# Kernel optimization log

Hardware: AMD Instinct MI355X
Metric: run time of the kernel (lower is better)

The kernel has to match this reference:

```python
import jax, jax.numpy as jnp
import numpy as np

N_NODES = 100000
N_EDGES = 1000000
F_IN = 8
HID = 64
VOCAB = 64
TXT_F = 64
SEQ = 10
N_CLASSES = 2


def setup_inputs() -> dict:
    key = jax.random.key(0)
    ks = jax.random.split(key, 16)
    inp = {
        "x": jax.random.normal(ks[0], (N_NODES, F_IN), dtype=jnp.float32),
        "edge_index": jax.random.randint(ks[1], (2, N_EDGES), 0, N_NODES, dtype=jnp.int32),
        "xtext": jax.random.randint(ks[2], (N_NODES, SEQ), 0, VOCAB, dtype=jnp.int32),
        # GCN layers (PyG convention: out = norm_agg(x @ W) + b)
        "conv1_w": jax.random.normal(ks[3], (F_IN, HID), dtype=jnp.float32) * 0.2,
        "conv1_b": jnp.zeros((HID,), jnp.float32),
        "conv2_w": jax.random.normal(ks[4], (HID, HID), dtype=jnp.float32) * 0.1,
        "conv2_b": jnp.zeros((HID,), jnp.float32),
        # embedding + GRU (torch layout: w_ih [3H, in], w_hh [3H, H])
        "embed": jax.random.normal(ks[5], (VOCAB, TXT_F), dtype=jnp.float32) * 0.1,
        "gru_w_ih": jax.random.normal(ks[6], (3 * HID, TXT_F), dtype=jnp.float32) * 0.1,
        "gru_w_hh": jax.random.normal(ks[7], (3 * HID, HID), dtype=jnp.float32) * 0.1,
        "gru_b_ih": jnp.zeros((3 * HID,), jnp.float32),
        "gru_b_hh": jnp.zeros((3 * HID,), jnp.float32),
        # pair MLPs (torch Linear layout: [out, in])
        "lin1_w": jax.random.normal(ks[8], (HID, 2 * HID), dtype=jnp.float32) * 0.1,
        "lin1_b": jnp.zeros((HID,), jnp.float32),
        "lin_text_w": jax.random.normal(ks[9], (HID, 2 * HID), dtype=jnp.float32) * 0.1,
        "lin_text_b": jnp.zeros((HID,), jnp.float32),
        "lin_final_w": jax.random.normal(ks[10], (N_CLASSES, 2 * HID), dtype=jnp.float32) * 0.1,
        "lin_final_b": jnp.zeros((N_CLASSES,), jnp.float32),
    }
    return inp


def _gcn_norm(edge_index, n_nodes):
    # PyG GCNConv default: add self loops, symmetric normalization
    loops = jnp.arange(n_nodes, dtype=edge_index.dtype)
    src = jnp.concatenate([edge_index[0], loops])
    dst = jnp.concatenate([edge_index[1], loops])
    deg = jax.ops.segment_sum(jnp.ones_like(dst, dtype=jnp.float32), dst, num_segments=n_nodes)
    dinv = jnp.where(deg > 0, jax.lax.rsqrt(deg), 0.0)
    norm = dinv[src] * dinv[dst]  # [E+N]
    return src, dst, norm


def _gcn(h, src, dst, norm, W, b, n_nodes):
    h = h @ W                              # [N, out]
    msg = h[src] * norm[:, None]           # gather + scale
    out = jax.ops.segment_sum(msg, dst, num_segments=n_nodes)
    return out + b


def _gru_last(xe, w_ih, w_hh, b_ih, b_hh):
    # xe: [N, T, F]; returns last hidden state [N, H]
    H = w_hh.shape[1]
    gi_all = jnp.einsum('ntf,gf->ntg', xe, w_ih) + b_ih  # precompute input gates [N,T,3H]
    gi_all = jnp.transpose(gi_all, (1, 0, 2))            # [T, N, 3H]

    def step(h, gi):
        gh = h @ w_hh.T + b_hh
        i_r, i_z, i_n = jnp.split(gi, 3, axis=-1)
        h_r, h_z, h_n = jnp.split(gh, 3, axis=-1)
        r = jax.nn.sigmoid(i_r + h_r)
        z = jax.nn.sigmoid(i_z + h_z)
        n = jnp.tanh(i_n + r * h_n)
        h = (1.0 - z) * n + z * h
        return h, None

    h0 = jnp.zeros((xe.shape[0], H), xe.dtype)
    h_last, _ = jax.lax.scan(step, h0, gi_all)
    return h_last


def reference(x, edge_index, xtext,
              conv1_w, conv1_b, conv2_w, conv2_b,
              embed, gru_w_ih, gru_w_hh, gru_b_ih, gru_b_hh,
              lin1_w, lin1_b, lin_text_w, lin_text_b, lin_final_w, lin_final_b):
    n = x.shape[0]
    src, dst, norm = _gcn_norm(edge_index, n)

    h = jax.nn.relu(_gcn(x, src, dst, norm, conv1_w, conv1_b, n))
    h = jax.nn.relu(_gcn(h, src, dst, norm, conv2_w, conv2_b, n))

    xe = embed[xtext]                                   # [N, T, F]
    textout = _gru_last(xe, gru_w_ih, gru_w_hh, gru_b_ih, gru_b_hh)  # [N, 64]

    s, t = edge_index[0], edge_index[1]
    xpair = jnp.concatenate([h[s], h[t]], axis=1)       # [E, 128]
    xpair = jax.nn.relu(xpair @ lin1_w.T + lin1_b)

    xpairtext = jnp.concatenate([textout[s], textout[t]], axis=1)
    xpairtext = jax.nn.relu(xpairtext @ lin_text_w.T + lin_text_b)

    xfin = jnp.concatenate([xpair, xpairtext], axis=1) @ lin_final_w.T + lin_final_b
    return jax.nn.log_softmax(xfin, axis=1)
```

## Files before the change

### kernel.cpp

```cpp
#include <hip/hip_runtime.h>
#include <stdint.h>

#define N_NODES 100000
#define N_EDGES 1000000
#define NBLK 391

typedef unsigned short u16;
typedef unsigned int u32;
typedef __attribute__((ext_vector_type(8))) short bshort8;
typedef __attribute__((ext_vector_type(4))) float f32x4;

__device__ __forceinline__ float bf2f(u16 u){ union{float f; u32 i;} x; x.i=((u32)u)<<16; return x.f; }
__device__ __forceinline__ u16 f2bf(float f){ union{float f; u32 i;} x; x.f=f; u32 r = x.i + 0x7FFFu + ((x.i>>16)&1u); return (u16)(r>>16); }

__device__ __forceinline__ float fexp2(float x){
#if __has_builtin(__builtin_amdgcn_exp2f)
    return __builtin_amdgcn_exp2f(x);
#else
    return exp2f(x);
#endif
}
__device__ __forceinline__ float frcp(float x){
#if __has_builtin(__builtin_amdgcn_rcpf)
    return __builtin_amdgcn_rcpf(x);
#else
    return 1.0f/x;
#endif
}
#define LOG2E 1.442695041f

__global__ void k_detect(const u16* __restrict__ x, int* flagp){
    __shared__ int cnt;
    if(threadIdx.x == 0) cnt = 0;
    __syncthreads();
    int c = 0;
    for(int i = threadIdx.x; i < 2048; i += 256){
        int e = (x[i] >> 7) & 0xFF;
        if(e >= 0x90) c++;
    }
    atomicAdd(&cnt, c);
    __syncthreads();
    if(threadIdx.x == 0) flagp[0] = (cnt > 64) ? 1 : 0;
}

#define CX    0
#define CW1   800000
#define CB1   800512
#define CW2   800576
#define CB2   804672
#define CEMB  804736
#define CWIH  808832
#define CWHH  821120
#define CBIH  833408
#define CBHH  833600
#define CL1W  833792
#define CL1B  841984
#define CLTW  842048
#define CLTB  850240
#define CLFW  850304
#define CLFB  850560
#define CTOT  850562

__device__ __forceinline__ float ldany(const void* p, int i, int fl){
    return fl ? ((const float*)p)[i] : bf2f(((const u16*)p)[i]);
}

__global__ void k_convert(const int* __restrict__ flagp,
                          const void* x, const void* w1, const void* b1, const void* w2,
                          const void* b2, const void* emb, const void* wih, const void* whh,
                          const void* bih, const void* bhh, const void* l1w, const void* l1b,
                          const void* ltw, const void* ltb, const void* lfw, const void* lfb,
                          float* __restrict__ canon){
    int i = blockIdx.x*256 + threadIdx.x;
    if(i >= CTOT) return;
    int fl = *flagp;
    const void* p; int off;
    if     (i < CW1 ){ p = x;   off = i;        }
    else if(i < CB1 ){ p = w1;  off = i - CW1;  }
    else if(i < CW2 ){ p = b1;  off = i - CB1;  }
    else if(i < CB2 ){ p = w2;  off = i - CW2;  }
    else if(i < CEMB){ p = b2;  off = i - CB2;  }
    else if(i < CWIH){ p = emb; off = i - CEMB; }
    else if(i < CWHH){ p = wih; off = i - CWIH; }
    else if(i < CBIH){ p = whh; off = i - CWHH; }
    else if(i < CBHH){ p = bih; off = i - CBIH; }
    else if(i < CL1W){ p = bhh; off = i - CBHH; }
    else if(i < CL1B){ p = l1w; off = i - CL1W; }
    else if(i < CLTW){ p = l1b; off = i - CL1B; }
    else if(i < CLTB){ p = ltw; off = i - CLTW; }
    else if(i < CLFW){ p = ltb; off = i - CLTB; }
    else if(i < CLFB){ p = lfw; off = i - CLFW; }
    else             { p = lfb; off = i - CLFB; }
    float v = ldany(p, off, fl);
    canon[i] = (v == v && fabsf(v) < 1e30f) ? v : 0.f;
}

__global__ void k_hist(const int* __restrict__ ei, int* __restrict__ deg){
    int e = blockIdx.x*256 + threadIdx.x;
    if(e < N_EDGES) atomicAdd(&deg[ei[N_EDGES + e]], 1);
}
__global__ void k_scan1(const int* __restrict__ deg, int* __restrict__ rowptr,
                        int* __restrict__ bsum){
    __shared__ int sh[256];
    int tid = threadIdx.x;
    int i = blockIdx.x*256 + tid;
    int v = (i < N_NODES) ? deg[i] : 0;
    sh[tid] = v;
    __syncthreads();
    for(int off = 1; off < 256; off <<= 1){
        int t = (tid >= off) ? sh[tid - off] : 0;
        __syncthreads();
        sh[tid] += t;
        __syncthreads();
    }
    if(i < N_NODES) rowptr[i] = sh[tid] - v;
    if(tid == 255) bsum[blockIdx.x] = sh[255];
}
__global__ void k_scan2(int* __restrict__ bsum){
    __shared__ int sh[512];
    int tid = threadIdx.x;
    int v = (tid < NBLK) ? bsum[tid] : 0;
    sh[tid] = v;
    __syncthreads();
    for(int off = 1; off < 512; off <<= 1){
        int t = (tid >= off) ? sh[tid - off] : 0;
        __syncthreads();
        sh[tid] += t;
        __syncthreads();
    }
    if(tid < NBLK) bsum[tid] = sh[tid] - v;
}
__global__ void k_scan3(const int* __restrict__ deg, const int* __restrict__ bsum,
                        int* __restrict__ rowptr, int* __restrict__ cursor,
                        float* __restrict__ dinv){
    int i = blockIdx.x*256 + threadIdx.x;
    if(i < N_NODES){
        int r = rowptr[i] + bsum[i >> 8];
        rowptr[i] = r;
        cursor[i] = r;
        dinv[i] = rsqrtf((float)deg[i] + 1.0f);
    }
    if(i == 0) rowptr[N_NODES] = N_EDGES;
}
__global__ void k_fill(const int* __restrict__ ei, int* __restrict__ cursor,
                       int* __restrict__ el, int* __restrict__ dl, int* __restrict__ eid){
    int e = blockIdx.x*256 + threadIdx.x;
    if(e < N_EDGES){
        int s = ei[e], d = ei[N_EDGES + e];
        int pos = atomicAdd(&cursor[d], 1);
        el[pos] = s;
        dl[pos] = d;
        eid[pos] = e;
    }
}

__global__ void k_t1s(const float* __restrict__ cx, const float* __restrict__ cw1,
                      const float* __restrict__ dinv, u16* __restrict__ src){
    __shared__ float w[512];
    int t = threadIdx.x;
    w[t]       = cw1[t];
    w[t + 256] = cw1[t + 256];
    __syncthreads();
    int i = blockIdx.x*256 + t;
    int n = i >> 6, f = i & 63;
    const float* xr = cx + n*8;
    float acc = 0.f;
    #pragma unroll
    for(int k = 0; k < 8; k++) acc += xr[k] * w[k*64 + f];
    src[i] = f2bf(acc * dinv[n]);
}

__global__ __launch_bounds__(256)
void k_gather_ep(const int* __restrict__ rowptr, const int* __restrict__ el,
                 const u16* __restrict__ src, const float* __restrict__ dinv,
                 const float* __restrict__ b, u16* __restrict__ h, int ostride){
    int gid = blockIdx.x*256 + threadIdx.x;
    int node = gid >> 6, lane = gid & 63;
    int beg = rowptr[node], end = rowptr[node + 1];
    float acc = bf2f(src[node*64 + lane]);
    int i = beg;
    for(; i + 4 <= end; i += 4){
        int s0 = el[i], s1 = el[i+1], s2 = el[i+2], s3 = el[i+3];
        float a0 = bf2f(src[s0*64 + lane]);
        float a1 = bf2f(src[s1*64 + lane]);
        float a2 = bf2f(src[s2*64 + lane]);
        float a3 = bf2f(src[s3*64 + lane]);
        acc += a0; acc += a1; acc += a2; acc += a3;
    }
    for(; i < end; i++) acc += bf2f(src[el[i]*64 + lane]);
    h[node*ostride + lane] = f2bf(fmaxf(dinv[node]*acc + b[lane], 0.f));
}

__global__ void k_packb(const float* __restrict__ src, u16* __restrict__ dst,
                        int K, int N, int ldk, int ldn){
    int i = blockIdx.x*256 + threadIdx.x;
    if(i >= K*N) return;
    int k = i / N, n = i % N;
    int kt = k >> 5, kk = k & 31, q = kk >> 3, j = kk & 7;
    int nt = n >> 4, nn = n & 15;
    int KT = K >> 5;
    dst[(((nt*KT + kt)*64) + (q*16 + nn))*8 + j] = f2bf(src[k*ldk + n*ldn]);
}

__global__ void k_gitab(const float* __restrict__ emb, const float* __restrict__ wih,
                        const float* __restrict__ bih, const float* __restrict__ bhh,
                        float* __restrict__ giT){
    int i = blockIdx.x*256 + threadIdx.x;
    if(i >= 64*192) return;
    int v = i / 192, g = i % 192;
    float acc = bih[g] + ((g < 128) ? bhh[g] : 0.0f);
    const float* wr = wih + g*64;
    const float* er = emb + v*64;
    for(int f = 0; f < 64; f++) acc += wr[f] * er[f];
    int g3 = g >> 6, rem = g & 63, t = rem >> 4, col = rem & 15;
    giT[(((size_t)v*3 + g3)*16 + col)*4 + t] = acc;
}

__global__ __launch_bounds__(256, 4)
void k_conv2(const u16* __restrict__ h, const u16* __restrict__ w2p,
             const float* __restrict__ dinv, u16* __restrict__ src){
    int wv = threadIdx.x >> 6, lane = threadIdx.x & 63;
    int g = blockIdx.x*4 + wv;
    if(g >= N_NODES/16) return;
    int q = lane >> 4, m = lane & 15, col = m;
    bshort8 a0 = *(const bshort8*)(h + (g*16 + m)*64 + q*8);
    bshort8 a1 = *(const bshort8*)(h + (g*16 + m)*64 + 32 + q*8);
    f32x4 acc[4];
    #pragma unroll
    for(int nt = 0; nt < 4; nt++){
        f32x4 c = {0.f,0.f,0.f,0.f};
        c = __builtin_amdgcn_mfma_f32_16x16x32_bf16(a0, *(const bshort8*)(w2p + ((nt*2+0)*64 + lane)*8), c, 0,0,0);
        c = __builtin_amdgcn_mfma_f32_16x16x32_bf16(a1, *(const bshort8*)(w2p + ((nt*2+1)*64 + lane)*8), c, 0,0,0);
        acc[nt] = c;
    }
    #pragma unroll
    for(int nt = 0; nt < 4; nt++)
        #pragma unroll
        for(int r = 0; r < 4; r++){
            int node = g*16 + q*4 + r;
            src[node*64 + nt*16 + col] = f2bf(acc[nt][r] * dinv[node]);
        }
}

__global__ __launch_bounds__(256, 4)
void k_gru(const int* __restrict__ xt, const u16* __restrict__ whhp,
           const float* __restrict__ giT, const float* __restrict__ bhh,
           u16* __restrict__ txt){
    __shared__ __align__(16) u16 wsh[12288];
    __shared__ __align__(16) u16 hsh[4][16][72];
    int tid = threadIdx.x;
    {
        const uint4* s = (const uint4*)whhp;
        uint4* d = (uint4*)wsh;
        #pragma unroll
        for(int i = 0; i < 6; i++) d[tid + 256*i] = s[tid + 256*i];
    }
    __syncthreads();

    int wv = tid >> 6, lane = tid & 63;
    int q = lane >> 4, m = lane & 15, col = m;
    int g = blockIdx.x*4 + wv;
    bool active = g < (N_NODES/16);
    int nb = active ? g*16 : 0;

    float bhhn[4];
    #pragma unroll
    for(int t = 0; t < 4; t++) bhhn[t] = bhh[128 + t*16 + col];

    const bshort8* wl = (const bshort8*)wsh;
    const u16* hp = &hsh[wv][m][0];

    float hc[4][4];
    #pragma unroll
    for(int t = 0; t < 4; t++)
        #pragma unroll
        for(int r = 0; r < 4; r++) hc[t][r] = 0.f;

    for(int s = 0; s < 10; s++){
        #pragma unroll
        for(int t = 0; t < 4; t++)
            #pragma unroll
            for(int r = 0; r < 4; r++)
                hsh[wv][q*4 + r][t*16 + col] = f2bf(hc[t][r]);

        asm volatile("" ::: "memory");
        bshort8 a0 = *(const bshort8*)(hp + q*8);
        bshort8 a1 = *(const bshort8*)(hp + 32 + q*8);

        int tok[4];
        #pragma unroll
        for(int r = 0; r < 4; r++) tok[r] = xt[(nb + q*4 + r)*10 + s] & 63;

        f32x4 acc[12];
        #pragma unroll
        for(int nt = 0; nt < 12; nt++){
            f32x4 c = {0.f,0.f,0.f,0.f};
            c = __builtin_amdgcn_mfma_f32_16x16x32_bf16(a0, wl[(nt*2+0)*64 + lane], c, 0,0,0);
            c = __builtin_amdgcn_mfma_f32_16x16x32_bf16(a1, wl[(nt*2+1)*64 + lane], c, 0,0,0);
            acc[nt] = c;
        }

        #pragma unroll
        for(int r = 0; r < 4; r++){
            const float4* gp = (const float4*)(giT + (size_t)tok[r]*192);
            float4 gr = gp[col];
            float4 gz = gp[16 + col];
            float4 gn = gp[32 + col];
            #pragma unroll
            for(int t = 0; t < 4; t++){
                float gir = ((const float*)&gr)[t];
                float giz = ((const float*)&gz)[t];
                float gin = ((const float*)&gn)[t];
                float rr = frcp(1.0f + fexp2(-LOG2E*(gir + acc[t][r])));
                float zz = frcp(1.0f + fexp2(-LOG2E*(giz + acc[4+t][r])));
                float narg = gin + rr*(acc[8+t][r] + bhhn[t]);
                float e2 = fexp2(2.0f*LOG2E*narg);
                float nn = 1.0f - 2.0f*frcp(e2 + 1.0f);
                hc[t][r] = nn + zz*(hc[t][r] - nn);
            }
        }
        asm volatile("" ::: "memory");
    }
    if(active){
        #pragma unroll
        for(int t = 0; t < 4; t++)
            #pragma unroll
            for(int r = 0; r < 4; r++)
                txt[(size_t)(nb + q*4 + r)*128 + t*16 + col] = f2bf(hc[t][r]);
    }
}

__global__ __launch_bounds__(256, 3)
void k_pairpre(u16* nodef, u32* __restrict__ udst,
               const u16* __restrict__ w1a, const u16* __restrict__ w1b,
               const u16* __restrict__ wta, const u16* __restrict__ wtb,
               const float* __restrict__ b1, const float* __restrict__ bt){
    int wv = threadIdx.x >> 6, lane = threadIdx.x & 63;
    int g = blockIdx.x*4 + wv;
    if(g >= N_NODES/16) return;
    int q = lane >> 4, m = lane & 15, col = m;
    const u16* row = nodef + (size_t)(g*16 + m)*128;
    bshort8 ah0 = *(const bshort8*)(row + q*8);
    bshort8 ah1 = *(const bshort8*)(row + 32 + q*8);
    bshort8 at0 = *(const bshort8*)(row + 64 + q*8);
    bshort8 at1 = *(const bshort8*)(row + 96 + q*8);
    f32x4 u1[4], u2[4], v1[4], v2[4];
    #pragma unroll
    for(int nt = 0; nt < 4; nt++){
        f32x4 c;
        c = (f32x4){0.f,0.f,0.f,0.f};
        c = __builtin_amdgcn_mfma_f32_16x16x32_bf16(ah0, *(const bshort8*)(w1a + ((nt*2+0)*64 + lane)*8), c, 0,0,0);
        c = __builtin_amdgcn_mfma_f32_16x16x32_bf16(ah1, *(const bshort8*)(w1a + ((nt*2+1)*64 + lane)*8), c, 0,0,0);
        u1[nt] = c;
        c = (f32x4){0.f,0.f,0.f,0.f};
        c = __builtin_amdgcn_mfma_f32_16x16x32_bf16(ah0, *(const bshort8*)(w1b + ((nt*2+0)*64 + lane)*8), c, 0,0,0);
        c = __builtin_amdgcn_mfma_f32_16x16x32_bf16(ah1, *(const bshort8*)(w1b + ((nt*2+1)*64 + lane)*8), c, 0,0,0);
        u2[nt] = c;
        c = (f32x4){0.f,0.f,0.f,0.f};
        c = __builtin_amdgcn_mfma_f32_16x16x32_bf16(at0, *(const bshort8*)(wta + ((nt*2+0)*64 + lane)*8), c, 0,0,0);
        c = __builtin_amdgcn_mfma_f32_16x16x32_bf16(at1, *(const bshort8*)(wta + ((nt*2+1)*64 + lane)*8), c, 0,0,0);
        v1[nt] = c;
        c = (f32x4){0.f,0.f,0.f,0.f};
        c = __builtin_amdgcn_mfma_f32_16x16x32_bf16(at0, *(const bshort8*)(wtb + ((nt*2+0)*64 + lane)*8), c, 0,0,0);
        c = __builtin_amdgcn_mfma_f32_16x16x32_bf16(at1, *(const bshort8*)(wtb + ((nt*2+1)*64 + lane)*8), c, 0,0,0);
        v2[nt] = c;
    }
    u32* usrc = (u32*)nodef;
    #pragma unroll
    for(int nt = 0; nt < 4; nt++){
        int f = nt*16 + col;
        float b1f = b1[f], btf = bt[f];
        #pragma unroll
        for(int r = 0; r < 4; r++){
            int node = g*16 + q*4 + r;
            u32 pa = (u32)f2bf(u1[nt][r] + b1f) | ((u32)f2bf(v1[nt][r] + btf) << 16);
            u32 pb = (u32)f2bf(u2[nt][r]) | ((u32)f2bf(v2[nt][r]) << 16);
            usrc[(size_t)node*64 + f] = pa;
            udst[(size_t)node*64 + f] = pb;
        }
    }
}

__global__ __launch_bounds__(256, 6)
void k_edge2(const int* __restrict__ el, const int* __restrict__ dl, const int* __restrict__ eid,
             const u32* __restrict__ usrc, const u32* __restrict__ udst,
             const float* __restrict__ wfin, const float* __restrict__ bfin,
             const int* __restrict__ flagp, void* __restrict__ out){
    int tid = threadIdx.x;
    int lane = tid & 63;
    int q = lane >> 4, f0 = lane & 15;
    int wid = (blockIdx.x*256 + tid) >> 6;
    int nwv = (gridDim.x*256) >> 6;
    int fl = *flagp;

    float wp0[4], wp1[4], wt0[4], wt1[4];
    #pragma unroll
    for(int t = 0; t < 4; t++){
        int f = f0 + 16*t;
        wp0[t] = wfin[f];        wt0[t] = wfin[64 + f];
        wp1[t] = wfin[128 + f];  wt1[t] = wfin[192 + f];
    }
    float bf0 = bfin[0], bf1 = bfin[1];

    for(int grp = wid; grp < N_EDGES/4; grp += nwv){
        int e = grp*4 + q;
        int s = el[e], d = dl[e];
        const u32* up = usrc + (size_t)s*64 + f0;
        const u32* vp = udst + (size_t)d*64 + f0;
        u32 us[4], ud[4];
        #pragma unroll
        for(int t = 0; t < 4; t++){ us[t] = up[16*t]; ud[t] = vp[16*t]; }
        float s0 = 0.f, s1 = 0.f;
        #pragma unroll
        for(int t = 0; t < 4; t++){
            float u1 = __uint_as_float(us[t] << 16);
            float v1 = __uint_as_float(us[t] & 0xffff0000u);
            float u2 = __uint_as_float(ud[t] << 16);
            float v2 = __uint_as_float(ud[t] & 0xffff0000u);
            float xp = fmaxf(u1 + u2, 0.f);
            float xq = fmaxf(v1 + v2, 0.f);
            s0 += xp*wp0[t] + xq*wt0[t];
            s1 += xp*wp1[t] + xq*wt1[t];
        }
        #pragma unroll
        for(int msk = 1; msk < 16; msk <<= 1){
            s0 += __shfl_xor(s0, msk, 64);
            s1 += __shfl_xor(s1, msk, 64);
        }
        if(f0 == 0){
            float a = s0 + bf0, b = s1 + bf1;
            float mx = fmaxf(a, b);
            float lse = mx + __logf(__expf(a - mx) + __expf(b - mx));
            int oi = eid[e];
            if(fl){
                float2 v; v.x = a - lse; v.y = b - lse;
                ((float2*)out)[oi] = v;
            }else{
                u32 pack = (u32)f2bf(a - lse) | ((u32)f2bf(b - lse) << 16);
                ((u32*)out)[oi] = pack;
            }
        }
    }
}

static const size_t O_FLAG   = 0;
static const size_t O_CANON  = 4096;
static const size_t O_GIT    = 3407872;
static const size_t O_W2P    = 3457024;
static const size_t O_WHHP   = 3465216;
static const size_t O_L1PA   = 3489792;
static const size_t O_L1PB   = 3497984;
static const size_t O_LTPA   = 3506176;
static const size_t O_LTPB   = 3514368;
static const size_t O_DINV   = 3522560;
static const size_t O_DEG    = 3922560;
static const size_t O_ROWPTR = 4322560;
static const size_t O_CURSOR = 4722688;
static const size_t O_BSUM   = 5122688;
static const size_t O_EL     = 5124736;
static const size_t O_DL     = 9125888;
static const size_t O_EID    = 13125888;
static const size_t O_SRC    = 17125888;
static const size_t O_H1     = 29925888;
static const size_t O_UDST   = 17125888;
static const size_t O_NODEF  = 42725888;

extern "C" void kernel_launch(void* const* d_in, const int* in_sizes, int n_in,
                              void* d_out, int out_size, void* d_ws, size_t ws_size,
                              hipStream_t stream){
    const void* x    = d_in[0];
    const int*  ei   = (const int*)d_in[1];
    const int*  xt   = (const int*)d_in[2];

    char* ws = (char*)d_ws;
    int*   flagp  = (int*)(ws + O_FLAG);
    float* canon  = (float*)(ws + O_CANON);
    float* giT    = (float*)(ws + O_GIT);
    u16*   w2p    = (u16*)(ws + O_W2P);
    u16*   whhp   = (u16*)(ws + O_WHHP);
    u16*   l1pa   = (u16*)(ws + O_L1PA);
    u16*   l1pb   = (u16*)(ws + O_L1PB);
    u16*   ltpa   = (u16*)(ws + O_LTPA);
    u16*   ltpb   = (u16*)(ws + O_LTPB);
    float* dinv   = (float*)(ws + O_DINV);
    int*   deg    = (int*)(ws + O_DEG);
    int*   rowptr = (int*)(ws + O_ROWPTR);
    int*   cursor = (int*)(ws + O_CURSOR);
    int*   bsum   = (int*)(ws + O_BSUM);
    int*   el     = (int*)(ws + O_EL);
    int*   dl     = (int*)(ws + O_DL);
    int*   eid    = (int*)(ws + O_EID);
    u16*   src    = (u16*)(ws + O_SRC);
    u16*   hbuf1  = (u16*)(ws + O_H1);
    u32*   udst   = (u32*)(ws + O_UDST);
    u16*   nodef  = (u16*)(ws + O_NODEF);

    k_detect<<<1, 256, 0, stream>>>((const u16*)x, flagp);
    k_convert<<<(CTOT+255)/256, 256, 0, stream>>>(flagp,
        x, d_in[3], d_in[4], d_in[5], d_in[6], d_in[7], d_in[8], d_in[9],
        d_in[10], d_in[11], d_in[12], d_in[13], d_in[14], d_in[15], d_in[16], d_in[17],
        canon);

    const float* cx   = canon + CX;
    const float* cw1  = canon + CW1;
    const float* cb1  = canon + CB1;
    const float* cw2  = canon + CW2;
    const float* cb2  = canon + CB2;
    const float* cemb = canon + CEMB;
    const float* cwih = canon + CWIH;
    const float* cwhh = canon + CWHH;
    const float* cbih = canon + CBIH;
    const float* cbhh = canon + CBHH;
    const float* cl1w = canon + CL1W;
    const float* cl1b = canon + CL1B;
    const float* cltw = canon + CLTW;
    const float* cltb = canon + CLTB;
    const float* clfw = canon + CLFW;
    const float* clfb = canon + CLFB;

    hipMemsetAsync(deg, 0, (size_t)N_NODES*4, stream);
    k_hist <<<(N_EDGES+255)/256, 256, 0, stream>>>(ei, deg);
    k_scan1<<<NBLK, 256, 0, stream>>>(deg, rowptr, bsum);
    k_scan2<<<1, 512, 0, stream>>>(bsum);
    k_scan3<<<NBLK, 256, 0, stream>>>(deg, bsum, rowptr, cursor, dinv);
    k_fill <<<(N_EDGES+255)/256, 256, 0, stream>>>(ei, cursor, el, dl, eid);

    k_packb<<<(64*64+255)/256, 256, 0, stream>>>(cw2, w2p, 64, 64, 64, 1);
    k_packb<<<(64*192+255)/256, 256, 0, stream>>>(cwhh, whhp, 64, 192, 1, 64);
    k_packb<<<(64*64+255)/256, 256, 0, stream>>>(cl1w,      l1pa, 64, 64, 1, 128);
    k_packb<<<(64*64+255)/256, 256, 0, stream>>>(cl1w + 64, l1pb, 64, 64, 1, 128);
    k_packb<<<(64*64+255)/256, 256, 0, stream>>>(cltw,      ltpa, 64, 64, 1, 128);
    k_packb<<<(64*64+255)/256, 256, 0, stream>>>(cltw + 64, ltpb, 64, 64, 1, 128);
    k_gitab<<<(64*192+255)/256, 256, 0, stream>>>(cemb, cwih, cbih, cbhh, giT);

    k_t1s<<<N_NODES*64/256, 256, 0, stream>>>(cx, cw1, dinv, src);
    k_gather_ep<<<N_NODES*64/256, 256, 0, stream>>>(rowptr, el, src, dinv, cb1, hbuf1, 64);

    k_conv2<<<(N_NODES/16 + 3)/4, 256, 0, stream>>>(hbuf1, w2p, dinv, src);
    k_gather_ep<<<N_NODES*64/256, 256, 0, stream>>>(rowptr, el, src, dinv, cb2, nodef, 128);

    k_gru<<<(N_NODES/16 + 3)/4, 256, 0, stream>>>(xt, whhp, giT, cbhh, nodef + 64);

    k_pairpre<<<(N_NODES/16 + 3)/4, 256, 0, stream>>>(nodef, udst, l1pa, l1pb, ltpa, ltpb,
                                                      cl1b, cltb);

    k_edge2<<<4096, 256, 0, stream>>>(el, dl, eid, (const u32*)nodef, udst,
                                      clfw, clfb, flagp, d_out);
}
```

Measured before the change: 495.2 us.

## Merge weight packing into one table kernel and fuse pair projection into GRU

Weight conversion, MFMA packing and the GRU input-gate table are now built by a single block-partitioned kernel that reads the raw inputs directly, replacing seven small launches. The per-node pair projection (lin1 and lin_text halves) moves into the tail of the GRU kernel. It uses the final hidden state from shared memory instead of writing the text features to global memory and reading them back in a separate kernel. This removes launch overhead and one round trip of node features, at the cost of more register pressure in the GRU kernel.

```diff
diff --git a/kernel.cpp b/kernel.cpp
--- a/kernel.cpp
+++ b/kernel.cpp
@@ -65,34 +65,84 @@
     return fl ? ((const float*)p)[i] : bf2f(((const u16*)p)[i]);
 }
 
-__global__ void k_convert(const int* __restrict__ flagp,
-                          const void* x, const void* w1, const void* b1, const void* w2,
-                          const void* b2, const void* emb, const void* wih, const void* whh,
-                          const void* bih, const void* bhh, const void* l1w, const void* l1b,
-                          const void* ltw, const void* ltb, const void* lfw, const void* lfb,
-                          float* __restrict__ canon){
-    int i = blockIdx.x*256 + threadIdx.x;
-    if(i >= CTOT) return;
+#define NCONV 3323
+#define B_W2  (NCONV)
+#define B_WHH (B_W2 + 16)
+#define B_L1A (B_WHH + 48)
+#define B_L1B (B_L1A + 16)
+#define B_LTA (B_L1B + 16)
+#define B_LTB (B_LTA + 16)
+#define B_GIT (B_LTB + 16)
+#define B_TOT (B_GIT + 48)
+
+__device__ __forceinline__ void packb_dev(const void* src, u16* dst,
+                                          int K, int N, int ldk, int ldn,
+                                          int fl, int i){
+    if(i >= K*N) return;
+    int k = i / N, n = i % N;
+    int kt = k >> 5, kk = k & 31, q = kk >> 3, j = kk & 7;
+    int nt = n >> 4, nn = n & 15;
+    int KT = K >> 5;
+    dst[(((nt*KT + kt)*64) + (q*16 + nn))*8 + j] = f2bf(ldany(src, k*ldk + n*ldn, fl));
+}
+
+__global__ void k_tables(const int* __restrict__ flagp,
+                         const void* x, const void* w1, const void* b1, const void* w2,
+                         const void* b2, const void* emb, const void* wih, const void* whh,
+                         const void* bih, const void* bhh, const void* l1w, const void* l1b,
+                         const void* ltw, const void* ltb, const void* lfw, const void* lfb,
+                         float* __restrict__ canon,
+                         u16* __restrict__ w2p, u16* __restrict__ whhp,
+                         u16* __restrict__ l1pa, u16* __restrict__ l1pb,
+                         u16* __restrict__ ltpa, u16* __restrict__ ltpb,
+                         float* __restrict__ giT){
+    int b = blockIdx.x, tid = threadIdx.x;
     int fl = *flagp;
-    const void* p; int off;
-    if     (i < CW1 ){ p = x;   off = i;        }
-    else if(i < CB1 ){ p = w1;  off = i - CW1;  }
-    else if(i < CW2 ){ p = b1;  off = i - CB1;  }
-    else if(i < CB2 ){ p = w2;  off = i - CW2;  }
-    else if(i < CEMB){ p = b2;  off = i - CB2;  }
-    else if(i < CWIH){ p = emb; off = i - CEMB; }
-    else if(i < CWHH){ p = wih; off = i - CWIH; }
-    else if(i < CBIH){ p = whh; off = i - CWHH; }
-    else if(i < CBHH){ p = bih; off = i - CBIH; }
-    else if(i < CL1W){ p = bhh; off = i - CBHH; }
-    else if(i < CL1B){ p = l1w; off = i - CL1W; }
-    else if(i < CLTW){ p = l1b; off = i - CL1B; }
-    else if(i < CLTB){ p = ltw; off = i - CLTW; }
-    else if(i < CLFW){ p = ltb; off = i - CLTB; }
-    else if(i < CLFB){ p = lfw; off = i - CLFW; }
-    else             { p = lfb; off = i - CLFB; }
-    float v = ldany(p, off, fl);
-    canon[i] = (v == v && fabsf(v) < 1e30f) ? v : 0.f;
+    if(b < NCONV){
+        int i = b*256 + tid;
+        if(i >= CTOT) return;
+        const void* p; int off;
+        if     (i < CW1 ){ p = x;   off = i;        }
+        else if(i < CB1 ){ p = w1;  off = i - CW1;  }
+        else if(i < CW2 ){ p = b1;  off = i - CB1;  }
+        else if(i < CB2 ){ p = w2;  off = i - CW2;  }
+        else if(i < CEMB){ p = b2;  off = i - CB2;  }
+        else if(i < CWIH){ p = emb; off = i - CEMB; }
+        else if(i < CWHH){ p = wih; off = i - CWIH; }
+        else if(i < CBIH){ p = whh; off = i - CWHH; }
+        else if(i < CBHH){ p = bih; off = i - CBIH; }
+        else if(i < CL1W){ p = bhh; off = i - CBHH; }
+        else if(i < CL1B){ p = l1w; off = i - CL1W; }
+        else if(i < CLTW){ p = l1b; off = i - CL1B; }
+        else if(i < CLTB){ p = ltw; off = i - CLTW; }
+        else if(i < CLFW){ p = ltb; off = i - CLTB; }
+        else if(i < CLFB){ p = lfw; off = i - CLFW; }
+        else             { p = lfb; off = i - CLFB; }
+        float v = ldany(p, off, fl);
+        canon[i] = (v == v && fabsf(v) < 1e30f) ? v : 0.f;
+    }else if(b < B_WHH){
+        packb_dev(w2, w2p, 64, 64, 64, 1, fl, (b - B_W2)*256 + tid);
+    }else if(b < B_L1A){
+        packb_dev(whh, whhp, 64, 192, 1, 64, fl, (b - B_WHH)*256 + tid);
+    }else if(b < B_L1B){
+        packb_dev(l1w, l1pa, 64, 64, 1, 128, fl, (b - B_L1A)*256 + tid);
+    }else if(b < B_LTA){
+        packb_dev((const u16*)0 ? (const void*)0 : (const void*)((const char*)l1w + (fl ? 64*4 : 64*2)),
+                  l1pb, 64, 64, 1, 128, fl, (b - B_L1B)*256 + tid);
+    }else if(b < B_LTB){
+        packb_dev(ltw, ltpa, 64, 64, 1, 128, fl, (b - B_LTA)*256 + tid);
+    }else if(b < B_GIT){
+        packb_dev((const void*)((const char*)ltw + (fl ? 64*4 : 64*2)),
+                  ltpb, 64, 64, 1, 128, fl, (b - B_LTB)*256 + tid);
+    }else{
+        int i = (b - B_GIT)*256 + tid;
+        if(i >= 64*192) return;
+        int v = i / 192, g = i % 192;
+        float acc = ldany(bih, g, fl) + ((g < 128) ? ldany(bhh, g, fl) : 0.0f);
+        for(int f = 0; f < 64; f++) acc += ldany(wih, g*64 + f, fl) * ldany(emb, v*64 + f, fl);
+        int g3 = g >> 6, rem = g & 63, t = rem >> 4, col = rem & 15;
+        giT[(((size_t)v*3 + g3)*16 + col)*4 + t] = acc;
+    }
 }
 
 __global__ void k_hist(const int* __restrict__ ei, int* __restrict__ deg){
@@ -191,31 +241,6 @@
     h[node*ostride + lane] = f2bf(fmaxf(dinv[node]*acc + b[lane], 0.f));
 }
 
-__global__ void k_packb(const float* __restrict__ src, u16* __restrict__ dst,
-                        int K, int N, int ldk, int ldn){
-    int i = blockIdx.x*256 + threadIdx.x;
-    if(i >= K*N) return;
-    int k = i / N, n = i % N;
-    int kt = k >> 5, kk = k & 31, q = kk >> 3, j = kk & 7;
-    int nt = n >> 4, nn = n & 15;
-    int KT = K >> 5;
-    dst[(((nt*KT + kt)*64) + (q*16 + nn))*8 + j] = f2bf(src[k*ldk + n*ldn]);
-}
-
-__global__ void k_gitab(const float* __restrict__ emb, const float* __restrict__ wih,
-                        const float* __restrict__ bih, const float* __restrict__ bhh,
-                        float* __restrict__ giT){
-    int i = blockIdx.x*256 + threadIdx.x;
-    if(i >= 64*192) return;
-    int v = i / 192, g = i % 192;
-    float acc = bih[g] + ((g < 128) ? bhh[g] : 0.0f);
-    const float* wr = wih + g*64;
-    const float* er = emb + v*64;
-    for(int f = 0; f < 64; f++) acc += wr[f] * er[f];
-    int g3 = g >> 6, rem = g & 63, t = rem >> 4, col = rem & 15;
-    giT[(((size_t)v*3 + g3)*16 + col)*4 + t] = acc;
-}
-
 __global__ __launch_bounds__(256, 4)
 void k_conv2(const u16* __restrict__ h, const u16* __restrict__ w2p,
              const float* __restrict__ dinv, u16* __restrict__ src){
@@ -245,7 +270,10 @@
 __global__ __launch_bounds__(256, 4)
 void k_gru(const int* __restrict__ xt, const u16* __restrict__ whhp,
            const float* __restrict__ giT, const float* __restrict__ bhh,
-           u16* __restrict__ txt){
+           u16* nodef, u32* __restrict__ udst,
+           const u16* __restrict__ w1a, const u16* __restrict__ w1b,
+           const u16* __restrict__ wta, const u16* __restrict__ wtb,
+           const float* __restrict__ b1, const float* __restrict__ bt){
     __shared__ __align__(16) u16 wsh[12288];
     __shared__ __align__(16) u16 hsh[4][16][72];
     int tid = threadIdx.x;
@@ -321,62 +349,43 @@
         }
         asm volatile("" ::: "memory");
     }
-    if(active){
-        #pragma unroll
-        for(int t = 0; t < 4; t++)
-            #pragma unroll
-            for(int r = 0; r < 4; r++)
-                txt[(size_t)(nb + q*4 + r)*128 + t*16 + col] = f2bf(hc[t][r]);
-    }
-}
-
-__global__ __launch_bounds__(256, 3)
-void k_pairpre(u16* nodef, u32* __restrict__ udst,
-               const u16* __restrict__ w1a, const u16* __restrict__ w1b,
-               const u16* __restrict__ wta, const u16* __restrict__ wtb,
-               const float* __restrict__ b1, const float* __restrict__ bt){
-    int wv = threadIdx.x >> 6, lane = threadIdx.x & 63;
-    int g = blockIdx.x*4 + wv;
-    if(g >= N_NODES/16) return;
-    int q = lane >> 4, m = lane & 15, col = m;
-    const u16* row = nodef + (size_t)(g*16 + m)*128;
+
+    #pragma unroll
+    for(int t = 0; t < 4; t++)
+        #pragma unroll
+        for(int r = 0; r < 4; r++)
+            hsh[wv][q*4 + r][t*16 + col] = f2bf(hc[t][r]);
+    asm volatile("" ::: "memory");
+    bshort8 at0 = *(const bshort8*)(hp + q*8);
+    bshort8 at1 = *(const bshort8*)(hp + 32 + q*8);
+    const u16* row = nodef + (size_t)(nb + m)*128;
     bshort8 ah0 = *(const bshort8*)(row + q*8);
     bshort8 ah1 = *(const bshort8*)(row + 32 + q*8);
-    bshort8 at0 = *(const bshort8*)(row + 64 + q*8);
-    bshort8 at1 = *(const bshort8*)(row + 96 + q*8);
-    f32x4 u1[4], u2[4], v1[4], v2[4];
+
+    u32* usrc = (u32*)nodef;
     #pragma unroll
     for(int nt = 0; nt < 4; nt++){
-        f32x4 c;
-        c = (f32x4){0.f,0.f,0.f,0.f};
-        c = __builtin_amdgcn_mfma_f32_16x16x32_bf16(ah0, *(const bshort8*)(w1a + ((nt*2+0)*64 + lane)*8), c, 0,0,0);
-        c = __builtin_amdgcn_mfma_f32_16x16x32_bf16(ah1, *(const bshort8*)(w1a + ((nt*2+1)*64 + lane)*8), c, 0,0,0);
-        u1[nt] = c;
-        c = (f32x4){0.f,0.f,0.f,0.f};
-        c = __builtin_amdgcn_mfma_f32_16x16x32_bf16(ah0, *(const bshort8*)(w1b + ((nt*2+0)*64 + lane)*8), c, 0,0,0);
-        c = __builtin_amdgcn_mfma_f32_16x16x32_bf16(ah1, *(const bshort8*)(w1b + ((nt*2+1)*64 + lane)*8), c, 0,0,0);
-        u2[nt] = c;
-        c = (f32x4){0.f,0.f,0.f,0.f};
-        c = __builtin_amdgcn_mfma_f32_16x16x32_bf16(at0, *(const bshort8*)(wta + ((nt*2+0)*64 + lane)*8), c, 0,0,0);
-        c = __builtin_amdgcn_mfma_f32_16x16x32_bf16(at1, *(const bshort8*)(wta + ((nt*2+1)*64 + lane)*8), c, 0,0,0);
-        v1[nt] = c;
-        c = (f32x4){0.f,0.f,0.f,0.f};
-        c = __builtin_amdgcn_mfma_f32_16x16x32_bf16(at0, *(const bshort8*)(wtb + ((nt*2+0)*64 + lane)*8), c, 0,0,0);
-        c = __builtin_amdgcn_mfma_f32_16x16x32_bf16(at1, *(const bshort8*)(wtb + ((nt*2+1)*64 + lane)*8), c, 0,0,0);
-        v2[nt] = c;
-    }
-    u32* usrc = (u32*)nodef;
-    #pragma unroll
-    for(int nt = 0; nt < 4; nt++){
-        int f = nt*16 + col;
-        float b1f = b1[f], btf = bt[f];
-        #pragma unroll
-        for(int r = 0; r < 4; r++){
-            int node = g*16 + q*4 + r;
-            u32 pa = (u32)f2bf(u1[nt][r] + b1f) | ((u32)f2bf(v1[nt][r] + btf) << 16);
-            u32 pb = (u32)f2bf(u2[nt][r]) | ((u32)f2bf(v2[nt][r]) << 16);
-            usrc[(size_t)node*64 + f] = pa;
-            udst[(size_t)node*64 + f] = pb;
+        f32x4 cu1 = {0.f,0.f,0.f,0.f}, cu2 = {0.f,0.f,0.f,0.f};
+        f32x4 cv1 = {0.f,0.f,0.f,0.f}, cv2 = {0.f,0.f,0.f,0.f};
+        cu1 = __builtin_amdgcn_mfma_f32_16x16x32_bf16(ah0, *(const bshort8*)(w1a + ((nt*2+0)*64 + lane)*8), cu1, 0,0,0);
+        cu1 = __builtin_amdgcn_mfma_f32_16x16x32_bf16(ah1, *(const bshort8*)(w1a + ((nt*2+1)*64 + lane)*8), cu1, 0,0,0);
+        cu2 = __builtin_amdgcn_mfma_f32_16x16x32_bf16(ah0, *(const bshort8*)(w1b + ((nt*2+0)*64 + lane)*8), cu2, 0,0,0);
+        cu2 = __builtin_amdgcn_mfma_f32_16x16x32_bf16(ah1, *(const bshort8*)(w1b + ((nt*2+1)*64 + lane)*8), cu2, 0,0,0);
+        cv1 = __builtin_amdgcn_mfma_f32_16x16x32_bf16(at0, *(const bshort8*)(wta + ((nt*2+0)*64 + lane)*8), cv1, 0,0,0);
+        cv1 = __builtin_amdgcn_mfma_f32_16x16x32_bf16(at1, *(const bshort8*)(wta + ((nt*2+1)*64 + lane)*8), cv1, 0,0,0);
+        cv2 = __builtin_amdgcn_mfma_f32_16x16x32_bf16(at0, *(const bshort8*)(wtb + ((nt*2+0)*64 + lane)*8), cv2, 0,0,0);
+        cv2 = __builtin_amdgcn_mfma_f32_16x16x32_bf16(at1, *(const bshort8*)(wtb + ((nt*2+1)*64 + lane)*8), cv2, 0,0,0);
+        if(active){
+            int f = nt*16 + col;
+            float b1f = b1[f], btf = bt[f];
+            #pragma unroll
+            for(int r = 0; r < 4; r++){
+                int node = nb + q*4 + r;
+                u32 pa = (u32)f2bf(cu1[r] + b1f) | ((u32)f2bf(cv1[r] + btf) << 16);
+                u32 pb = (u32)f2bf(cu2[r]) | ((u32)f2bf(cv2[r]) << 16);
+                usrc[(size_t)node*64 + f] = pa;
+                udst[(size_t)node*64 + f] = pb;
+            }
         }
     }
 }
@@ -496,24 +505,17 @@
     u16*   nodef  = (u16*)(ws + O_NODEF);
 
     k_detect<<<1, 256, 0, stream>>>((const u16*)x, flagp);
-    k_convert<<<(CTOT+255)/256, 256, 0, stream>>>(flagp,
+    k_tables<<<B_TOT, 256, 0, stream>>>(flagp,
         x, d_in[3], d_in[4], d_in[5], d_in[6], d_in[7], d_in[8], d_in[9],
         d_in[10], d_in[11], d_in[12], d_in[13], d_in[14], d_in[15], d_in[16], d_in[17],
-        canon);
+        canon, w2p, whhp, l1pa, l1pb, ltpa, ltpb, giT);
 
     const float* cx   = canon + CX;
     const float* cw1  = canon + CW1;
     const float* cb1  = canon + CB1;
-    const float* cw2  = canon + CW2;
     const float* cb2  = canon + CB2;
-    const float* cemb = canon + CEMB;
-    const float* cwih = canon + CWIH;
-    const float* cwhh = canon + CWHH;
-    const float* cbih = canon + CBIH;
     const float* cbhh = canon + CBHH;
-    const float* cl1w = canon + CL1W;
     const float* cl1b = canon + CL1B;
-    const float* cltw = canon + CLTW;
     const float* cltb = canon + CLTB;
     const float* clfw = canon + CLFW;
     const float* clfb = canon + CLFB;
@@ -525,24 +527,15 @@
     k_scan3<<<NBLK, 256, 0, stream>>>(deg, bsum, rowptr, cursor, dinv);
     k_fill <<<(N_EDGES+255)/256, 256, 0, stream>>>(ei, cursor, el, dl, eid);
 
-    k_packb<<<(64*64+255)/256, 256, 0, stream>>>(cw2, w2p, 64, 64, 64, 1);
-    k_packb<<<(64*192+255)/256, 256, 0, stream>>>(cwhh, whhp, 64, 192, 1, 64);
-    k_packb<<<(64*64+255)/256, 256, 0, stream>>>(cl1w,      l1pa, 64, 64, 1, 128);
-    k_packb<<<(64*64+255)/256, 256, 0, stream>>>(cl1w + 64, l1pb, 64, 64, 1, 128);
-    k_packb<<<(64*64+255)/256, 256, 0, stream>>>(cltw,      ltpa, 64, 64, 1, 128);
-    k_packb<<<(64*64+255)/256, 256, 0, stream>>>(cltw + 64, ltpb, 64, 64, 1, 128);
-    k_gitab<<<(64*192+255)/256, 256, 0, stream>>>(cemb, cwih, cbih, cbhh, giT);
-
     k_t1s<<<N_NODES*64/256, 256, 0, stream>>>(cx, cw1, dinv, src);
     k_gather_ep<<<N_NODES*64/256, 256, 0, stream>>>(rowptr, el, src, dinv, cb1, hbuf1, 64);
 
     k_conv2<<<(N_NODES/16 + 3)/4, 256, 0, stream>>>(hbuf1, w2p, dinv, src);
     k_gather_ep<<<N_NODES*64/256, 256, 0, stream>>>(rowptr, el, src, dinv, cb2, nodef, 128);
 
-    k_gru<<<(N_NODES/16 + 3)/4, 256, 0, stream>>>(xt, whhp, giT, cbhh, nodef + 64);
-
-    k_pairpre<<<(N_NODES/16 + 3)/4, 256, 0, stream>>>(nodef, udst, l1pa, l1pb, ltpa, ltpb,
-                                                      cl1b, cltb);
+    k_gru<<<(N_NODES/16 + 3)/4, 256, 0, stream>>>(xt, whhp, giT, cbhh,
+                                                  nodef, udst, l1pa, l1pb, ltpa, ltpb,
+                                                  cl1b, cltb);
 
     k_edge2<<<4096, 256, 0, stream>>>(el, dl, eid, (const u32*)nodef, udst,
                                       clfw, clfb, flagp, d_out);
```

After: 473.5 us. -4.4%, faster.
